# Kernel optimization log

Hardware: AMD Instinct MI355X
Metric: run time of the kernel (lower is better)

The kernel has to match this reference:

```python
import jax, jax.numpy as jnp
import numpy as np

HEADS = 16
DIM_HEAD = 64
QUERY_DIM = 1024
CONTEXT_DIM = 1024
D_ATTN = HEADS * DIM_HEAD
SCALE = DIM_HEAD ** -0.5


def setup_inputs() -> dict:
    key = jax.random.key(0)
    ks = jax.random.split(key, 7)
    B, N, M = 4, 2048, 1024
    x = jax.random.normal(ks[0], (B, N, QUERY_DIM), dtype=jnp.float32)
    context = jax.random.normal(ks[1], (B, M, CONTEXT_DIM), dtype=jnp.float32)
    # Linear weights stored as [in, out] (no bias for Q/K/V, bias for to_out)
    s = 0.02
    Wq = jax.random.normal(ks[2], (QUERY_DIM, D_ATTN), dtype=jnp.float32) * s
    Wk = jax.random.normal(ks[3], (CONTEXT_DIM, D_ATTN), dtype=jnp.float32) * s
    Wv = jax.random.normal(ks[4], (CONTEXT_DIM, D_ATTN), dtype=jnp.float32) * s
    Wo = jax.random.normal(ks[5], (D_ATTN, QUERY_DIM), dtype=jnp.float32) * s
    bo = jax.random.normal(ks[6], (QUERY_DIM,), dtype=jnp.float32) * s
    return {"x": x, "context": context, "Wq": Wq, "Wk": Wk, "Wv": Wv, "Wo": Wo, "bo": bo}


def reference(x, context, Wq, Wk, Wv, Wo, bo):
    B, N, _ = x.shape
    M = context.shape[1]
    Q = (x @ Wq).reshape(B, N, HEADS, DIM_HEAD)        # b n h d
    K = (context @ Wk).reshape(B, M, HEADS, DIM_HEAD)  # b m h d
    V = (context @ Wv).reshape(B, M, HEADS, DIM_HEAD)
    # scores: b q h m  (matches torch einsum 'bqhd,bhmd->bqhm')
    scores = jnp.einsum('bqhd,bmhd->bqhm', Q, K) * SCALE
    attn = jax.nn.softmax(scores, axis=-1)
    out = jnp.einsum('bqhm,bmhd->bqhd', attn, V)
    out = out.reshape(B, N, D_ATTN)
    return out @ Wo + bo  # dropout p=0.0 -> identity
```

## Files before the change

kernel.cpp:

```cpp
#include <hip/hip_runtime.h>
#include <math.h>


#define HEADS 16
#define DHEAD 64
#define DM    1024
#define BQ    4
#define NQ    2048
#define MK    1024

typedef unsigned short u16;
typedef __attribute__((ext_vector_type(8))) short bf16x8;
typedef __attribute__((ext_vector_type(4))) float f32x4;
typedef __attribute__((ext_vector_type(16))) float f32x16;

__device__ __forceinline__ u16 f2bf(float f) {
  unsigned u = __builtin_bit_cast(unsigned, f);
  u = u + 0x7FFFu + ((u >> 16) & 1u);
  return (u16)(u >> 16);
}

__device__ __forceinline__ unsigned cvtpk(float lo, float hi2) {
  unsigned r;
  asm("v_cvt_pk_bf16_f32 %0, %1, %2" : "=v"(r) : "v"(lo), "v"(hi2));
  return r;
}

__device__ __forceinline__ float max3f(float a, float b, float c) {
  float d;
  asm("v_max3_f32 %0, %1, %2, %3" : "=v"(d) : "v"(a), "v"(b), "v"(c));
  return d;
}

__device__ __forceinline__ void gld16(const u16* g, u16* l) {
  __builtin_amdgcn_global_load_lds((const __attribute__((address_space(1))) void*)g,
                                   (__attribute__((address_space(3))) void*)l,
                                   16, 0, 0);
}

__global__ void k_cvt(const float* __restrict__ in, u16* __restrict__ out, int n8) {
  int i = blockIdx.x * 256 + threadIdx.x;
  if (i >= n8) return;
  float4 a = ((const float4*)in)[i * 2];
  float4 b = ((const float4*)in)[i * 2 + 1];
  union { u16 h[8]; int4 v; } r;
  r.h[0] = f2bf(a.x); r.h[1] = f2bf(a.y); r.h[2] = f2bf(a.z); r.h[3] = f2bf(a.w);
  r.h[4] = f2bf(b.x); r.h[5] = f2bf(b.y); r.h[6] = f2bf(b.z); r.h[7] = f2bf(b.w);
  ((int4*)out)[i] = r.v;
}

__global__ void k_wt(const float* __restrict__ W0, const float* __restrict__ W1,
                     const float* __restrict__ W2, const float* __restrict__ W3,
                     u16* __restrict__ out) {
  __shared__ float t[32][33];
  const float* W = blockIdx.z == 0 ? W0 : blockIdx.z == 1 ? W1 : blockIdx.z == 2 ? W2 : W3;
  u16* o = out + (size_t)blockIdx.z * DM * DM;
  int r0 = blockIdx.y * 32, c0 = blockIdx.x * 32;
  int tx = threadIdx.x, ty = threadIdx.y;
  for (int i = ty; i < 32; i += 8) t[i][tx] = W[(size_t)(r0 + i) * DM + c0 + tx];
  __syncthreads();
  for (int i = ty; i < 32; i += 8) o[(size_t)(c0 + i) * DM + r0 + tx] = f2bf(t[tx][i]);
}


#define STG2(buf, k0) do {                               \
  gld16(gA0 + (k0), &As[buf][w * 512]);                  \
  gld16(gA1 + (k0), &As[buf][4096 + w * 512]);           \
  gld16(gB0 + (k0), &Bs[buf][w * 512]);                  \
} while (0)

#define GEMM2_COMPUTE(cur) do {                                                          \
  bf16x8 af[4], bfr[4];                                                                  \
  _Pragma("unroll")                                                                      \
  for (int mi = 0; mi < 4; mi++)                                                         \
    af[mi]  = *(const bf16x8*)&As[cur][(wr * 64 + mi * 16 + lrow) * 32 + sl];            \
  _Pragma("unroll")                                                                      \
  for (int ni = 0; ni < 4; ni++)                                                         \
    bfr[ni] = *(const bf16x8*)&Bs[cur][(wc * 64 + ni * 16 + lrow) * 32 + sl];            \
  __builtin_amdgcn_s_setprio(1);                                                         \
  _Pragma("unroll")                                                                      \
  for (int mi = 0; mi < 4; mi++)                                                         \
    _Pragma("unroll")                                                                    \
    for (int ni = 0; ni < 4; ni++)                                                       \
      acc[mi][ni] = __builtin_amdgcn_mfma_f32_16x16x32_bf16(af[mi], bfr[ni],             \
                                                            acc[mi][ni], 0, 0, 0);      \
  __builtin_amdgcn_s_setprio(0);                                                         \
} while (0)

#define GEMM2_LOOP() do {                                      \
  STG2(0, 0);                                                  \
  _Pragma("unroll 2")                                          \
  for (int kt = 0; kt < 32; ++kt) {                            \
    int cur = kt & 1;                                          \
    if (kt < 31) {                                             \
      STG2(cur ^ 1, (kt + 1) * 32);                            \
      asm volatile("s_waitcnt vmcnt(3)" ::: "memory");         \
    } else {                                                   \
      asm volatile("s_waitcnt vmcnt(0)" ::: "memory");         \
    }                                                          \
    __builtin_amdgcn_s_barrier();                              \
    __builtin_amdgcn_sched_barrier(0);                         \
    GEMM2_COMPUTE(cur);                                        \
    __builtin_amdgcn_sched_barrier(0);                         \
    __builtin_amdgcn_s_barrier();                              \
    __builtin_amdgcn_sched_barrier(0);                         \
  }                                                            \
} while (0)

__global__ __launch_bounds__(512, 2) void k_gemm_qkv(const u16* __restrict__ xb,
                                                     const u16* __restrict__ cb,
                                                     const u16* __restrict__ wt,
                                                     u16* __restrict__ Qb,
                                                     u16* __restrict__ Kb,
                                                     u16* __restrict__ Vtb) {
  __shared__ u16 As[2][8192];
  __shared__ u16 Bs[2][4096];
  int lin = blockIdx.x;
  int swz = (lin & 7) * 64 + (lin >> 3);
  int p = swz >> 3, bx = swz & 7;
  const u16* A; const u16* Bt; u16* obf; int row0, mode;
  if (p < 32)      { A = xb; Bt = wt;           obf = Qb;  row0 = p * 256;        mode = 0; }
  else if (p < 48) { A = cb; Bt = wt + 1048576; obf = Kb;  row0 = (p - 32) * 256; mode = 0; }
  else             { A = cb; Bt = wt + 2097152; obf = Vtb; row0 = (p - 48) * 256; mode = 1; }
  int col0 = bx * 128;
  int t = threadIdx.x;
  int w = t >> 6, lane = t & 63, lrow = lane & 15, lgrp = lane >> 4;
  int wr = w >> 1, wc = w & 1;
  int sl = (lgrp ^ (lrow & 3)) * 8;
  f32x4 acc[4][4] = {};
  int srow = t >> 2;
  int scol = ((t & 3) ^ (srow & 3)) * 8;
  const u16* gA0 = A  + (size_t)(row0 + srow) * DM + scol;
  const u16* gA1 = gA0 + (size_t)128 * DM;
  const u16* gB0 = Bt + (size_t)(col0 + srow) * DM + scol;

  GEMM2_LOOP();

  #pragma unroll
  for (int mi = 0; mi < 4; mi++)
    #pragma unroll
    for (int ni = 0; ni < 4; ni++)
      #pragma unroll
      for (int j = 0; j < 4; j++) {
        int gr = row0 + wr * 64 + mi * 16 + lgrp * 4 + j;
        int gc = col0 + wc * 64 + ni * 16 + lrow;
        float v = acc[mi][ni][j];
        if (mode == 0) {
          obf[(size_t)gr * DM + gc] = f2bf(v);
        } else {
          int b = gr >> 10, m = gr & 1023;
          obf[((size_t)(b * DM + gc)) * MK + m] = f2bf(v);
        }
      }
}

__global__ __launch_bounds__(512, 2) void k_gemm_o(const u16* __restrict__ A,
                                                   const u16* __restrict__ Bt,
                                                   float* __restrict__ of32,
                                                   const float* __restrict__ bias) {
  __shared__ u16 As[2][8192];
  __shared__ u16 Bs[2][4096];
  int lin = blockIdx.x;
  int swz = (lin & 7) * 32 + (lin >> 3);
  int p = swz >> 3, bx = swz & 7;
  int row0 = p * 256, col0 = bx * 128;
  int t = threadIdx.x;
  int w = t >> 6, lane = t & 63, lrow = lane & 15, lgrp = lane >> 4;
  int wr = w >> 1, wc = w & 1;
  int sl = (lgrp ^ (lrow & 3)) * 8;
  f32x4 acc[4][4] = {};
  int srow = t >> 2;
  int scol = ((t & 3) ^ (srow & 3)) * 8;
  const u16* gA0 = A  + (size_t)(row0 + srow) * DM + scol;
  const u16* gA1 = gA0 + (size_t)128 * DM;
  const u16* gB0 = Bt + (size_t)(col0 + srow) * DM + scol;

  GEMM2_LOOP();

  #pragma unroll
  for (int mi = 0; mi < 4; mi++)
    #pragma unroll
    for (int ni = 0; ni < 4; ni++)
      #pragma unroll
      for (int j = 0; j < 4; j++) {
        int gr = row0 + wr * 64 + mi * 16 + lgrp * 4 + j;
        int gc = col0 + wc * 64 + ni * 16 + lrow;
        of32[(size_t)gr * DM + gc] = acc[mi][ni][j] + bias[gc];
      }
}

#define BUILD_PFRAG(sv, base, frag) {                     \
  unsigned a_ = cvtpk(sv[base + 0], sv[base + 1]);        \
  unsigned c_ = cvtpk(sv[base + 2], sv[base + 3]);        \
  unsigned b_ = cvtpk(sv[base + 4], sv[base + 5]);        \
  unsigned d_ = cvtpk(sv[base + 6], sv[base + 7]);        \
  unsigned y1 = hi ? a_ : b_;                             \
  unsigned y2 = hi ? c_ : d_;                             \
  unsigned x1 = (unsigned)__shfl_xor((int)y1, 32);        \
  unsigned x2 = (unsigned)__shfl_xor((int)y2, 32);        \
  union { unsigned w[4]; bf16x8 v; } u_;                  \
  u_.w[0] = hi ? x1 : a_;  u_.w[1] = hi ? x2 : c_;        \
  u_.w[2] = hi ? b_ : x1;  u_.w[3] = hi ? d_ : x2;        \
  frag = u_.v; }

#define PV_CHUNK(sv, base, c) {                                               \
  bf16x8 pf_; BUILD_PFRAG(sv, base, pf_);                                     \
  int mo_ = ((c) * 16 + hi * 8) ^ sw;                                         \
  bf16x8 vf0_ = *(const bf16x8*)&Vl[ln * 64 + mo_];                           \
  bf16x8 vf1_ = *(const bf16x8*)&Vl[(32 + ln) * 64 + mo_];                    \
  __builtin_amdgcn_s_setprio(1);                                              \
  o0 = __builtin_amdgcn_mfma_f32_32x32x16_bf16(vf0_, pf_, o0, 0, 0, 0);       \
  o1 = __builtin_amdgcn_mfma_f32_32x32x16_bf16(vf1_, pf_, o1, 0, 0, 0);       \
  __builtin_amdgcn_s_setprio(0); }

__device__ __forceinline__ float max16(const f32x16 &v) {
  float m0 = max3f(v[0], v[1], v[2]);
  float m1 = max3f(v[3], v[4], v[5]);
  float m2 = max3f(v[6], v[7], v[8]);
  float m3 = max3f(v[9], v[10], v[11]);
  float m4 = max3f(v[12], v[13], v[14]);
  float a = max3f(m0, m1, m2);
  float b = max3f(m3, m4, v[15]);
  return fmaxf(a, b);
}

__device__ __forceinline__ float sum16(const f32x16 &v) {
  float a = (v[0] + v[1]) + (v[2] + v[3]);
  float b = (v[4] + v[5]) + (v[6] + v[7]);
  float c = (v[8] + v[9]) + (v[10] + v[11]);
  float d = (v[12] + v[13]) + (v[14] + v[15]);
  return (a + b) + (c + d);
}

__global__ __launch_bounds__(512) void k_attn(const u16* __restrict__ Q,
                                              const u16* __restrict__ K,
                                              const u16* __restrict__ Vt,
                                              u16* __restrict__ O) {
  __shared__ __align__(16) u16 Kl[4096];
  __shared__ __align__(16) u16 Vl[4096];
  int bh = blockIdx.y, b = bh >> 4, h = bh & 15;
  int n0 = blockIdx.x * 256;
  int t = threadIdx.x, w = t >> 6, lane = t & 63;
  int ln = lane & 31, hi = lane >> 5;
  const float s2 = 0.18033688011112042f;

  int qrow = n0 + w * 32 + ln;
  const u16* qp = &Q[(((size_t)(b * NQ + qrow)) * HEADS + h) * DHEAD + hi * 8];
  bf16x8 qf0 = *(const bf16x8*)(qp);
  bf16x8 qf1 = *(const bf16x8*)(qp + 16);
  bf16x8 qf2 = *(const bf16x8*)(qp + 32);
  bf16x8 qf3 = *(const bf16x8*)(qp + 48);

  f32x16 o0 = {}, o1 = {};
  float M_ = -1e30f, L_ = 0.f;

  int srow = t >> 3, sp = (t & 7) * 8;
  const u16* kg = &K[(((size_t)(b * MK + srow)) * HEADS + h) * DHEAD + sp];
  const u16* vg = &Vt[((size_t)(b * DM) + h * DHEAD + srow) * MK + sp];
  int sd = srow * 64 + (sp ^ ((srow & 7) << 3));
  int sw = (ln & 7) << 3;

  int4 kv = *(const int4*)kg;
  int4 vv = *(const int4*)vg;

  for (int it = 0; it < 16; ++it) {
    __syncthreads();
    *(int4*)&Kl[sd] = kv;
    *(int4*)&Vl[sd] = vv;
    __syncthreads();
    if (it < 15) {
      kv = *(const int4*)(kg + (size_t)(it + 1) * (64 * HEADS * DHEAD));
      vv = *(const int4*)(vg + (it + 1) * 64);
    }

    f32x16 s0 = {}, s1 = {};
    __builtin_amdgcn_s_setprio(1);
    #pragma unroll
    for (int kd = 0; kd < 4; ++kd) {
      int doff = (kd * 16 + hi * 8) ^ sw;
      bf16x8 kf0 = *(const bf16x8*)&Kl[ln * 64 + doff];
      bf16x8 kf1 = *(const bf16x8*)&Kl[(32 + ln) * 64 + doff];
      bf16x8 qk = kd == 0 ? qf0 : kd == 1 ? qf1 : kd == 2 ? qf2 : qf3;
      s0 = __builtin_amdgcn_mfma_f32_32x32x16_bf16(kf0, qk, s0, 0, 0, 0);
      s1 = __builtin_amdgcn_mfma_f32_32x32x16_bf16(kf1, qk, s1, 0, 0, 0);
    }
    __builtin_amdgcn_s_setprio(0);

    float vm = fmaxf(max16(s0), max16(s1));

    if (!__all(vm - M_ <= 8.0f)) {
      float vm2 = fmaxf(vm, __shfl_xor(vm, 32));
      float mn = fmaxf(M_, vm2);
      float rc = exp2f((M_ - mn) * s2);
      M_ = mn;
      L_ *= rc;
      #pragma unroll
      for (int i = 0; i < 16; ++i) { o0[i] *= rc; o1[i] *= rc; }
    }
    float nb = M_ * s2;
    #pragma unroll
    for (int i = 0; i < 16; ++i) s0[i] = exp2f(s0[i] * s2 - nb);
    #pragma unroll
    for (int i = 0; i < 16; ++i) s1[i] = exp2f(s1[i] * s2 - nb);
    L_ += sum16(s0) + sum16(s1);

    PV_CHUNK(s0, 0, 0);
    PV_CHUNK(s0, 8, 1);
    PV_CHUNK(s1, 0, 2);
    PV_CHUNK(s1, 8, 3);
  }

  float Lt = L_ + __shfl_xor(L_, 32);
  float inv = 1.0f / Lt;
  u16* ob = (u16*)&O[(((size_t)(b * NQ + qrow)) * HEADS + h) * DHEAD];
  #pragma unroll
  for (int g = 0; g < 4; ++g) {
    union { u16 h4[4]; uint2 v; } r0, r1;
    #pragma unroll
    for (int s = 0; s < 4; ++s) {
      r0.h4[s] = f2bf(o0[4 * g + s] * inv);
      r1.h4[s] = f2bf(o1[4 * g + s] * inv);
    }
    *(uint2*)(ob + 8 * g + 4 * hi) = r0.v;
    *(uint2*)(ob + 32 + 8 * g + 4 * hi) = r1.v;
  }
}

extern "C" void kernel_launch(void* const* d_in, const int* in_sizes, int n_in,
                              void* d_out, int out_size, void* d_ws, size_t ws_size,
                              hipStream_t stream) {
  (void)in_sizes; (void)n_in; (void)out_size; (void)ws_size;
  const float* x   = (const float*)d_in[0];
  const float* ctx = (const float*)d_in[1];
  const float* Wq  = (const float*)d_in[2];
  const float* Wk  = (const float*)d_in[3];
  const float* Wv  = (const float*)d_in[4];
  const float* Wo  = (const float*)d_in[5];
  const float* bo  = (const float*)d_in[6];
  float* out = (float*)d_out;
  char* ws = (char*)d_ws;
  const size_t MB = 1u << 20;
  u16* xb  = (u16*)(ws);
  u16* cb  = (u16*)(ws + 16 * MB);
  u16* wt  = (u16*)(ws + 24 * MB);
  u16* Qb  = (u16*)(ws + 32 * MB);
  u16* Kb  = (u16*)(ws + 48 * MB);
  u16* Vtb = (u16*)(ws + 56 * MB);
  u16* Ab  = (u16*)(ws + 64 * MB);

  k_cvt<<<4096, 256, 0, stream>>>(x,   xb, 1048576);
  k_cvt<<<2048, 256, 0, stream>>>(ctx, cb, 524288);
  k_wt<<<dim3(32, 32, 4), dim3(32, 8), 0, stream>>>(Wq, Wk, Wv, Wo, wt);

  k_gemm_qkv<<<512, 512, 0, stream>>>(xb, cb, wt, Qb, Kb, Vtb);

  k_attn<<<dim3(8, 64), 512, 0, stream>>>(Qb, Kb, Vtb, Ab);

  k_gemm_o<<<256, 512, 0, stream>>>(Ab, wt + 3145728, out, bo);
}
```

Measured before the change: 182.4 us.

## Double-buffer K/V shared tiles and use permlane32 swap for P fragments

The K and V shared-memory tiles become double-buffered. The next tile is written into the alternate buffer after the PV MFMAs, so each iteration needs one barrier instead of two, and global-load latency can overlap compute. The cross-half P fragment exchange also replaces two shuffles plus selects with v_permlane32_swap instructions. This doubles LDS usage per block, which may reduce occupancy.

```diff
diff --git a/kernel.cpp b/kernel.cpp
--- a/kernel.cpp
+++ b/kernel.cpp
@@ -194,20 +194,18 @@
   unsigned c_ = cvtpk(sv[base + 2], sv[base + 3]);        \
   unsigned b_ = cvtpk(sv[base + 4], sv[base + 5]);        \
   unsigned d_ = cvtpk(sv[base + 6], sv[base + 7]);        \
-  unsigned y1 = hi ? a_ : b_;                             \
-  unsigned y2 = hi ? c_ : d_;                             \
-  unsigned x1 = (unsigned)__shfl_xor((int)y1, 32);        \
-  unsigned x2 = (unsigned)__shfl_xor((int)y2, 32);        \
+  asm("v_permlane32_swap_b32 %0, %1" : "+v"(a_), "+v"(b_)); \
+  asm("v_permlane32_swap_b32 %0, %1" : "+v"(c_), "+v"(d_)); \
   union { unsigned w[4]; bf16x8 v; } u_;                  \
-  u_.w[0] = hi ? x1 : a_;  u_.w[1] = hi ? x2 : c_;        \
-  u_.w[2] = hi ? b_ : x1;  u_.w[3] = hi ? d_ : x2;        \
+  u_.w[0] = a_;  u_.w[1] = c_;                            \
+  u_.w[2] = b_;  u_.w[3] = d_;                            \
   frag = u_.v; }
 
 #define PV_CHUNK(sv, base, c) {                                               \
   bf16x8 pf_; BUILD_PFRAG(sv, base, pf_);                                     \
   int mo_ = ((c) * 16 + hi * 8) ^ sw;                                         \
-  bf16x8 vf0_ = *(const bf16x8*)&Vl[ln * 64 + mo_];                           \
-  bf16x8 vf1_ = *(const bf16x8*)&Vl[(32 + ln) * 64 + mo_];                    \
+  bf16x8 vf0_ = *(const bf16x8*)&Vlc[ln * 64 + mo_];                          \
+  bf16x8 vf1_ = *(const bf16x8*)&Vlc[(32 + ln) * 64 + mo_];                   \
   __builtin_amdgcn_s_setprio(1);                                              \
   o0 = __builtin_amdgcn_mfma_f32_32x32x16_bf16(vf0_, pf_, o0, 0, 0, 0);       \
   o1 = __builtin_amdgcn_mfma_f32_32x32x16_bf16(vf1_, pf_, o1, 0, 0, 0);       \
@@ -236,8 +234,8 @@
                                               const u16* __restrict__ K,
                                               const u16* __restrict__ Vt,
                                               u16* __restrict__ O) {
-  __shared__ __align__(16) u16 Kl[4096];
-  __shared__ __align__(16) u16 Vl[4096];
+  __shared__ __align__(16) u16 Kl[2][4096];
+  __shared__ __align__(16) u16 Vl[2][4096];
   int bh = blockIdx.y, b = bh >> 4, h = bh & 15;
   int n0 = blockIdx.x * 256;
   int t = threadIdx.x, w = t >> 6, lane = t & 63;
@@ -262,12 +260,14 @@
 
   int4 kv = *(const int4*)kg;
   int4 vv = *(const int4*)vg;
+  *(int4*)&Kl[0][sd] = kv;
+  *(int4*)&Vl[0][sd] = vv;
+  __syncthreads();
 
   for (int it = 0; it < 16; ++it) {
-    __syncthreads();
-    *(int4*)&Kl[sd] = kv;
-    *(int4*)&Vl[sd] = vv;
-    __syncthreads();
+    int cur = it & 1;
+    const u16* Klc = Kl[cur];
+    const u16* Vlc = Vl[cur];
     if (it < 15) {
       kv = *(const int4*)(kg + (size_t)(it + 1) * (64 * HEADS * DHEAD));
       vv = *(const int4*)(vg + (it + 1) * 64);
@@ -278,8 +278,8 @@
     #pragma unroll
     for (int kd = 0; kd < 4; ++kd) {
       int doff = (kd * 16 + hi * 8) ^ sw;
-      bf16x8 kf0 = *(const bf16x8*)&Kl[ln * 64 + doff];
-      bf16x8 kf1 = *(const bf16x8*)&Kl[(32 + ln) * 64 + doff];
+      bf16x8 kf0 = *(const bf16x8*)&Klc[ln * 64 + doff];
+      bf16x8 kf1 = *(const bf16x8*)&Klc[(32 + ln) * 64 + doff];
       bf16x8 qk = kd == 0 ? qf0 : kd == 1 ? qf1 : kd == 2 ? qf2 : qf3;
       s0 = __builtin_amdgcn_mfma_f32_32x32x16_bf16(kf0, qk, s0, 0, 0, 0);
       s1 = __builtin_amdgcn_mfma_f32_32x32x16_bf16(kf1, qk, s1, 0, 0, 0);
@@ -308,6 +308,12 @@
     PV_CHUNK(s0, 8, 1);
     PV_CHUNK(s1, 0, 2);
     PV_CHUNK(s1, 8, 3);
+
+    if (it < 15) {
+      *(int4*)&Kl[cur ^ 1][sd] = kv;
+      *(int4*)&Vl[cur ^ 1][sd] = vv;
+    }
+    __syncthreads();
   }
 
   float Lt = L_ + __shfl_xor(L_, 32);
```

New measurement: 175.6 us. 3.7% less time.
